# Kernel optimization log

Hardware: AMD Instinct MI355X
Metric: run time of the kernel (lower is better)

The kernel has to match this reference:

```python
import jax, jax.numpy as jnp
import numpy as np

N = 1 << 20
L, F, T = 16, 2, 1 << 19          # levels, feats/level, hashmap size
BASE, DESIRED = 16, 2048
PLANE_RES, PF = 512, 8
APP_COUNT, APP_DIM = 1024, 48
GEO = 15
_b = np.exp((np.log(DESIRED) - np.log(BASE)) / (L - 1))
RES = np.floor(BASE * _b ** np.arange(L)).astype(np.float32)   # per-level grid res
PRIMES = np.array([1, 2654435761, 805459861], dtype=np.uint32)
CORNERS = np.stack(np.meshgrid(*[[0, 1]] * 3, indexing='ij'), -1).reshape(8, 3)
PAIRS = np.array([[0, 1], [0, 2], [1, 2]])


def hash_encode(pos01, tables):
    # pos01: [N,3] in [0,1]; tables: [L,T,F]
    corners_u = jnp.asarray(CORNERS, jnp.uint32)
    corners_b = jnp.asarray(CORNERS, bool)
    primes = jnp.asarray(PRIMES)

    def level(table, R):
        p = pos01 * R                      # [N,3]
        pf = jnp.floor(p)
        fr = p - pf                        # trilinear weights
        pi = pf.astype(jnp.uint32)
        corner = pi[:, None, :] + corners_u            # [N,8,3]
        h = corner * primes                            # uint32 wraps (mod 2^32)
        idx = (h[..., 0] ^ h[..., 1] ^ h[..., 2]) & jnp.uint32(T - 1)
        w = jnp.prod(jnp.where(corners_b, fr[:, None, :], 1.0 - fr[:, None, :]), axis=-1)
        return jnp.einsum('nkf,nk->nf', table[idx], w)  # [N,F]

    feats = jax.vmap(level)(tables, jnp.asarray(RES))   # [L,N,F]
    return jnp.moveaxis(feats, 0, 1).reshape(pos01.shape[0], L * F)


def plane_encode(pos01, planes):
    # planes: [3, R, R, PF]; bilinear interp on (xy, xz, yz) projections
    outs = []
    for i in range(3):
        uv = pos01[:, PAIRS[i]] * (PLANE_RES - 1)
        uf = jnp.floor(uv)
        fr = uv - uf
        ui = jnp.clip(uf.astype(jnp.int32), 0, PLANE_RES - 2)
        u0, v0 = ui[:, 0], ui[:, 1]
        pl = planes[i]
        wu, wv = fr[:, 0:1], fr[:, 1:2]
        f = (pl[u0, v0] * (1 - wu) * (1 - wv) + pl[u0, v0 + 1] * (1 - wu) * wv
             + pl[u0 + 1, v0] * wu * (1 - wv) + pl[u0 + 1, v0 + 1] * wu * wv)
        outs.append(f)
    return jnp.concatenate(outs, -1)   # [N, 3*PF]


def sh_encode(d):
    # degree-4 real spherical harmonics (torch-ngp convention), d normalized
    x, y, z = d[:, 0], d[:, 1], d[:, 2]
    xx, yy, zz = x * x, y * y, z * z
    xy, yz, xz = x * y, y * z, x * z
    return jnp.stack([
        0.28209479177387814 * jnp.ones_like(x),
        -0.48860251190291987 * y, 0.48860251190291987 * z, -0.48860251190291987 * x,
        1.0925484305920792 * xy, -1.0925484305920792 * yz,
        0.94617469575755997 * zz - 0.31539156525252005,
        -1.0925484305920792 * xz, 0.5462742152960396 * (xx - yy),
        -0.5900435899266435 * y * (3 * xx - yy), 2.890611442640554 * xy * z,
        -0.4570457994644658 * y * (4 * zz - xx - yy),
        0.3731763325901154 * z * (2 * zz - 3 * xx - 3 * yy),
        -0.4570457994644658 * x * (4 * zz - xx - yy),
        1.445305721320277 * z * (xx - yy),
        -0.5900435899266435 * x * (xx - 3 * yy)], axis=-1)


def setup_inputs() -> dict:
    key = jax.random.key(0)
    ks = jax.random.split(key, 10)
    pos = jax.random.uniform(ks[0], (N, 3), jnp.float32, -1.0, 1.0)
    dirs = jax.random.normal(ks[1], (N, 3), jnp.float32)
    dirs = dirs / jnp.linalg.norm(dirs, axis=-1, keepdims=True)
    app = jax.random.randint(ks[2], (N, 1), 0, APP_COUNT).astype(jnp.float32)
    x = jnp.concatenate([pos, dirs, app], -1)
    hash_tables = jax.random.uniform(ks[3], (L, T, F), jnp.float32, -1e-4, 1e-4)
    planes = jax.random.normal(ks[4], (3, PLANE_RES, PLANE_RES, PF), jnp.float32) * 0.1
    embed_a = jax.random.normal(ks[5], (APP_COUNT, APP_DIM), jnp.float32)

    def lin(k, o, i):
        return jax.random.normal(k, (o, i), jnp.float32) * np.float32(np.sqrt(2.0 / i))
    return {
        'x': x, 'hash_tables': hash_tables, 'planes': planes, 'embed_a': embed_a,
        'w_sigma0': lin(ks[6], 64, L * F + 3 * PF),
        'w_sigma1': lin(ks[7], 1 + GEO, 64),
        'w_color0': lin(ks[8], 64, 16 + GEO + APP_DIM + 3 * PF),
        'w_color1': lin(ks[9], 64, 64),
        'w_color2': lin(jax.random.fold_in(key, 99), 3, 64),
    }


def reference(x, hash_tables, planes, embed_a, w_sigma0, w_sigma1, w_color0, w_color1, w_color2):
    pos01 = (x[:, :3] + 1.0) * 0.5            # bound = 1 -> [0,1]
    h = hash_encode(pos01, hash_tables)       # [N,32]
    pf = plane_encode(pos01, planes)          # [N,24]
    h = jnp.concatenate([h, pf], -1)
    h = jax.nn.relu(h @ w_sigma0.T)
    h = h @ w_sigma1.T                        # [N,16]
    sigma = jnp.exp(jnp.clip(h[..., 0], -15.0, 15.0))   # trunc_exp
    geo = h[..., 1:]
    d = x[:, 3:6]
    d = d / jnp.linalg.norm(d, axis=-1, keepdims=True)
    sh = sh_encode(d)                         # [N,16]
    a = embed_a[x[:, -1].astype(jnp.int32)]   # [N,48]
    hc = jnp.concatenate([sh, geo, a, pf], -1)
    hc = jax.nn.relu(hc @ w_color0.T)
    hc = jax.nn.relu(hc @ w_color1.T)
    color = jax.nn.sigmoid(hc @ w_color2.T)
    return jnp.concatenate([color, sigma[:, None]], -1)   # [N,4]
```

## Files before the change

### kernel.cpp

```cpp
#include <hip/hip_runtime.h>
#include <cmath>
#include <stdint.h>

#define NLEV  16
#define TSIZE (1u<<19)
#define PRES  512
#define PFD   8
#define HID   64
#define LDSH  72

struct ResArr { float v[NLEV]; };

typedef __attribute__((ext_vector_type(8))) short short8v;
typedef __attribute__((ext_vector_type(4))) float f32x4;

__device__ __forceinline__ float4 ld4(const float* p){ return *reinterpret_cast<const float4*>(p); }

__device__ __forceinline__ uint16_t f2bf(float f){
    uint32_t u = __float_as_uint(f);
    uint32_t r = (u + 0x7FFFu + ((u>>16)&1u)) >> 16;
    return (uint16_t)r;
}
__device__ __forceinline__ float bf2f(uint32_t h){ return __uint_as_float(h<<16); }

#define AXPY64(A, WPTR, V) do { const float* _w=(WPTR); const float _v=(V); \
  _Pragma("unroll") \
  for (int _o=0;_o<64;_o+=4){ float4 _w4=ld4(_w+_o); \
    A[_o+0]=fmaf(_w4.x,_v,A[_o+0]); A[_o+1]=fmaf(_w4.y,_v,A[_o+1]); \
    A[_o+2]=fmaf(_w4.z,_v,A[_o+2]); A[_o+3]=fmaf(_w4.w,_v,A[_o+3]); } } while(0)

__device__ __forceinline__ void plane_enc(const float* __restrict__ planes,
                                          float p0, float p1, float p2, float* pfv)
{
#pragma unroll
    for (int i=0;i<3;i++){
        float ua = (i==2? p1 : p0)*511.f;
        float va = (i==0? p1 : p2)*511.f;
        float uf=floorf(ua), vf=floorf(va);
        float wu=ua-uf, wv=va-vf;
        int u0=(int)uf; u0 = u0<0?0:(u0>510?510:u0);
        int v0=(int)vf; v0 = v0<0?0:(v0>510?510:v0);
        const float* pl = planes + ((size_t)i*PRES*PRES + (size_t)(u0*PRES+v0))*PFD;
        float4 a0=ld4(pl),              a1=ld4(pl+4);
        float4 b0=ld4(pl+PFD),          b1=ld4(pl+PFD+4);
        float4 c0=ld4(pl+PRES*PFD),     c1=ld4(pl+PRES*PFD+4);
        float4 d0=ld4(pl+PRES*PFD+PFD), d1=ld4(pl+PRES*PFD+PFD+4);
        float w00=(1.f-wu)*(1.f-wv), w01=(1.f-wu)*wv, w10=wu*(1.f-wv), w11=wu*wv;
        pfv[i*8+0]=a0.x*w00+b0.x*w01+c0.x*w10+d0.x*w11;
        pfv[i*8+1]=a0.y*w00+b0.y*w01+c0.y*w10+d0.y*w11;
        pfv[i*8+2]=a0.z*w00+b0.z*w01+c0.z*w10+d0.z*w11;
        pfv[i*8+3]=a0.w*w00+b0.w*w01+c0.w*w10+d0.w*w11;
        pfv[i*8+4]=a1.x*w00+b1.x*w01+c1.x*w10+d1.x*w11;
        pfv[i*8+5]=a1.y*w00+b1.y*w01+c1.y*w10+d1.y*w11;
        pfv[i*8+6]=a1.z*w00+b1.z*w01+c1.z*w10+d1.z*w11;
        pfv[i*8+7]=a1.w*w00+b1.w*w01+c1.w*w10+d1.w*w11;
    }
}

__global__ void nerf_krepack(const float2* __restrict__ tabs,
                             uint32_t* __restrict__ tabs_bf, int total)
{
    int i = blockIdx.x*256 + threadIdx.x;
    if (i < total){
        float2 t = tabs[i];
        tabs_bf[i] = (uint32_t)f2bf(t.x) | ((uint32_t)f2bf(t.y)<<16);
    }
}

__global__ void nerf_kprep(const float* __restrict__ x, float4* __restrict__ pp, int npts)
{
    int n = blockIdx.x*256 + threadIdx.x;
    if (n < npts){
        const float* xr = x + (size_t)n*7;
        pp[n] = make_float4((xr[0]+1.f)*0.5f, (xr[1]+1.f)*0.5f, (xr[2]+1.f)*0.5f, xr[6]);
    }
}

__global__ __launch_bounds__(256, 2)
void nerf_k0b(const float4* __restrict__ pp,
              const uint32_t* __restrict__ tabs_bf,
              uint32_t* __restrict__ feat,
              ResArr res, int npts, int lvl_base)
{
    int bid   = blockIdx.x;
    int level = lvl_base + (bid & 7);
    int chunk = bid >> 3;
    int base_n = chunk*2048 + threadIdx.x;
    float R = res.v[level];
    const uint32_t* tab = tabs_bf + (size_t)level*TSIZE;

    uint32_t g[8][8];
    float rx[8], ry[8], rz[8];
#pragma unroll
    for (int q=0;q<8;q++){
        int n = base_n + q*256;
        int nc = (n < npts) ? n : 0;
        float4 p = pp[nc];
        float ax=p.x*R, ay=p.y*R, az=p.z*R;
        float fx=floorf(ax), fy=floorf(ay), fz=floorf(az);
        rx[q]=ax-fx; ry[q]=ay-fy; rz[q]=az-fz;
        uint32_t ix=(uint32_t)fx, iy=(uint32_t)fy, iz=(uint32_t)fz;
        uint32_t hx0=ix,             hx1=ix+1u;
        uint32_t hy0=iy*2654435761u, hy1=(iy+1u)*2654435761u;
        uint32_t hz0=iz*805459861u,  hz1=(iz+1u)*805459861u;
#pragma unroll
        for (int c=0;c<8;c++){
            uint32_t idx = (((c&4)?hx1:hx0) ^ ((c&2)?hy1:hy0) ^ ((c&1)?hz1:hz0)) & (TSIZE-1u);
            g[q][c] = tab[idx];
        }
    }
#pragma unroll
    for (int q=0;q<8;q++){
        float wx0=1.f-rx[q], wy0=1.f-ry[q], wz0=1.f-rz[q];
        float f0=0.f, f1=0.f;
#pragma unroll
        for (int c=0;c<8;c++){
            float w = ((c&4)?rx[q]:wx0)*((c&2)?ry[q]:wy0)*((c&1)?rz[q]:wz0);
            f0 = fmaf(w, bf2f(g[q][c] & 0xFFFFu), f0);
            f1 = fmaf(w, bf2f(g[q][c] >> 16),     f1);
        }
        int n = base_n + q*256;
        if (n < npts) feat[(size_t)level*npts + n] = (uint32_t)f2bf(f0) | ((uint32_t)f2bf(f1)<<16);
    }
}

__global__ __launch_bounds__(256, 2)
void nerf_k0(const float* __restrict__ x,
             const float* __restrict__ hash_tables,
             uint32_t* __restrict__ feat,
             ResArr res, int npts, int lvl_base)
{
    int bid   = blockIdx.x;
    int level = lvl_base + (bid & 7);
    int chunk = bid >> 3;
    int n0 = chunk*512 + threadIdx.x;
    int n1 = n0 + 256;
    float R = res.v[level];
    const float2* tab = reinterpret_cast<const float2*>(hash_tables) + (size_t)level*TSIZE;

    bool v0ok = (n0 < npts), v1ok = (n1 < npts);

    float p0a=0,p1a=0,p2a=0, p0b=0,p1b=0,p2b=0;
    if (v0ok){ const float* xr = x + (size_t)n0*7;
        p0a=(xr[0]+1.f)*0.5f; p1a=(xr[1]+1.f)*0.5f; p2a=(xr[2]+1.f)*0.5f; }
    if (v1ok){ const float* xr = x + (size_t)n1*7;
        p0b=(xr[0]+1.f)*0.5f; p1b=(xr[1]+1.f)*0.5f; p2b=(xr[2]+1.f)*0.5f; }

    float axa=p0a*R, aya=p1a*R, aza=p2a*R;
    float fxa=floorf(axa), fya=floorf(aya), fza=floorf(aza);
    float rxa=axa-fxa, rya=aya-fya, rza=aza-fza;
    uint32_t ixa=(uint32_t)fxa, iya=(uint32_t)fya, iza=(uint32_t)fza;
    uint32_t hx0a=ixa,             hx1a=ixa+1u;
    uint32_t hy0a=iya*2654435761u, hy1a=(iya+1u)*2654435761u;
    uint32_t hz0a=iza*805459861u,  hz1a=(iza+1u)*805459861u;

    float axb=p0b*R, ayb=p1b*R, azb=p2b*R;
    float fxb=floorf(axb), fyb=floorf(ayb), fzb=floorf(azb);
    float rxb=axb-fxb, ryb=ayb-fyb, rzb=azb-fzb;
    uint32_t ixb=(uint32_t)fxb, iyb=(uint32_t)fyb, izb=(uint32_t)fzb;
    uint32_t hx0b=ixb,             hx1b=ixb+1u;
    uint32_t hy0b=iyb*2654435761u, hy1b=(iyb+1u)*2654435761u;
    uint32_t hz0b=izb*805459861u,  hz1b=(izb+1u)*805459861u;

    float2 ta[8], tb[8];
#pragma unroll
    for (int c=0;c<8;c++){
        uint32_t idx = (((c&4)?hx1a:hx0a) ^ ((c&2)?hy1a:hy0a) ^ ((c&1)?hz1a:hz0a)) & (TSIZE-1u);
        ta[c] = tab[idx];
    }
#pragma unroll
    for (int c=0;c<8;c++){
        uint32_t idx = (((c&4)?hx1b:hx0b) ^ ((c&2)?hy1b:hy0b) ^ ((c&1)?hz1b:hz0b)) & (TSIZE-1u);
        tb[c] = tab[idx];
    }

    float wxa0=1.f-rxa, wya0=1.f-rya, wza0=1.f-rza;
    float f0a=0.f, f1a=0.f;
#pragma unroll
    for (int c=0;c<8;c++){
        float w = ((c&4)?rxa:wxa0)*((c&2)?rya:wya0)*((c&1)?rza:wza0);
        f0a = fmaf(w,ta[c].x,f0a); f1a = fmaf(w,ta[c].y,f1a);
    }
    float wxb0=1.f-rxb, wyb0=1.f-ryb, wzb0=1.f-rzb;
    float f0b=0.f, f1b=0.f;
#pragma unroll
    for (int c=0;c<8;c++){
        float w = ((c&4)?rxb:wxb0)*((c&2)?ryb:wyb0)*((c&1)?rzb:wzb0);
        f0b = fmaf(w,tb[c].x,f0b); f1b = fmaf(w,tb[c].y,f1b);
    }

    size_t base = (size_t)level*npts;
    if (v0ok) feat[base+n0] = (uint32_t)f2bf(f0a) | ((uint32_t)f2bf(f1a)<<16);
    if (v1ok) feat[base+n1] = (uint32_t)f2bf(f0b) | ((uint32_t)f2bf(f1b)<<16);
}

__global__ void nerf_ktrans(const float* __restrict__ w_sigma0,
                            const float* __restrict__ w_sigma1,
                            const float* __restrict__ w_color0,
                            const float* __restrict__ w_color1,
                            const float* __restrict__ w_color2,
                            float* __restrict__ t_s0, float* __restrict__ t_s1,
                            float* __restrict__ t_c2,
                            short* __restrict__ c0Bhi, short* __restrict__ c0Blo,
                            short* __restrict__ c1Bhi, short* __restrict__ c1Blo,
                            short* __restrict__ s0Bhi, short* __restrict__ s0Blo,
                            short* __restrict__ s1Bhi, short* __restrict__ s1Blo,
                            short* __restrict__ c2Bhi, short* __restrict__ c2Blo)
{
    int tid = threadIdx.x;
    for (int i=tid;i<56*64; i+=256){ int k=i>>6,o=i&63; t_s0[i]=w_sigma0[o*56+k]; }
    for (int i=tid;i<64*16; i+=256){ int k=i>>4,j=i&15; t_s1[i]=w_sigma1[j*64+k]; }
    for (int i=tid;i<64*4;  i+=256){ int k=i>>2,o=i&3;  t_c2[i]=(o<3)?w_color2[o*64+k]:0.f; }

    for (int idx=tid; idx<4096; idx+=256){
        int nt = idx >> 10;
        int r1 = idx & 1023;
        int ks = r1 >> 9;
        int r2 = r1 & 511;
        int l  = r2 >> 3;
        int i  = r2 & 7;
        int out = nt*16 + (l & 15);
        int kk  = ks*32 + (l >> 4)*8 + i;
        float w0 = 0.f;
        if (kk < 31)       w0 = w_color0[out*103 + kk];
        else if (kk < 55)  w0 = w_color0[out*103 + kk + 48];
        uint16_t h0 = f2bf(w0);
        uint16_t l0 = f2bf(w0 - bf2f(h0));
        c0Bhi[idx] = (short)h0; c0Blo[idx] = (short)l0;
        float w1 = w_color1[out*64 + kk];
        uint16_t h1 = f2bf(w1);
        uint16_t l1 = f2bf(w1 - bf2f(h1));
        c1Bhi[idx] = (short)h1; c1Blo[idx] = (short)l1;
        float ws = (kk < 56) ? w_sigma0[out*56 + kk] : 0.f;
        uint16_t hs = f2bf(ws);
        uint16_t ls = f2bf(ws - bf2f(hs));
        s0Bhi[idx] = (short)hs; s0Blo[idx] = (short)ls;
    }
    for (int idx=tid; idx<1024; idx+=256){
        int ks = idx >> 9;
        int r2 = idx & 511;
        int l  = r2 >> 3;
        int i  = r2 & 7;
        int out = l & 15;
        int kk  = ks*32 + (l >> 4)*8 + i;
        float w = w_sigma1[out*64 + kk];
        uint16_t h = f2bf(w);
        s1Bhi[idx] = (short)h; s1Blo[idx] = (short)f2bf(w - bf2f(h));
        float wc = (out < 3) ? w_color2[out*64 + kk] : 0.f;
        uint16_t hc2 = f2bf(wc);
        c2Bhi[idx] = (short)hc2; c2Blo[idx] = (short)f2bf(wc - bf2f(hc2));
    }
}

__global__ void nerf_kpre(const float* __restrict__ embed_a,
                          const float* __restrict__ w_color0,
                          float* __restrict__ app_pre)
{
    int a = blockIdx.x;
    int o = threadIdx.x;
    const float* er = embed_a + (size_t)a*48;
    const float* wr = w_color0 + (size_t)o*103 + 31;
    float s = 0.f;
#pragma unroll
    for (int j=0;j<48;j++) s = fmaf(er[j], wr[j], s);
    app_pre[(size_t)a*64 + o] = s;
}

__global__ __launch_bounds__(256, 2)
void nerf_k1s(const float* __restrict__ x,
              const float* __restrict__ planes,
              uint32_t* __restrict__ feat,
              const float* __restrict__ wT_s0,
              const float* __restrict__ wT_s1,
              int npts)
{
    int n = blockIdx.x*256 + threadIdx.x;
    if (n >= npts) return;

    uint32_t fl[NLEV];
#pragma unroll
    for (int l=0;l<NLEV;l++) fl[l] = feat[(size_t)l*npts + n];

    float acc[HID];
#pragma unroll
    for (int o=0;o<HID;o++) acc[o]=0.f;

#pragma unroll
    for (int l=0;l<NLEV;l++){
        float f0 = bf2f(fl[l] & 0xFFFFu);
        float f1 = bf2f(fl[l] >> 16);
        AXPY64(acc, &wT_s0[(2*l+0)*64], f0);
        AXPY64(acc, &wT_s0[(2*l+1)*64], f1);
    }

    const float* xr = x + (size_t)n*7;
    float p0=(xr[0]+1.f)*0.5f, p1=(xr[1]+1.f)*0.5f, p2=(xr[2]+1.f)*0.5f;
    float pfv[24];
    plane_enc(planes, p0, p1, p2, pfv);
#pragma unroll
    for (int j=0;j<24;j++){
        AXPY64(acc, &wT_s0[(32+j)*64], pfv[j]);
    }

    float h1[16];
#pragma unroll
    for (int j=0;j<16;j++) h1[j]=0.f;
#pragma unroll
    for (int k=0;k<HID;k++){
        float v = fmaxf(acc[k], 0.f);
        const float* wr = &wT_s1[k*16];
#pragma unroll
        for (int j=0;j<16;j+=4){
            float4 w=ld4(wr+j);
            h1[j+0]=fmaf(w.x,v,h1[j+0]); h1[j+1]=fmaf(w.y,v,h1[j+1]);
            h1[j+2]=fmaf(w.z,v,h1[j+2]); h1[j+3]=fmaf(w.w,v,h1[j+3]);
        }
    }
    float sg = fminf(fmaxf(h1[0], -15.f), 15.f);
    float sigma = expf(sg);

#pragma unroll
    for (int l=0;l<15;l++) feat[(size_t)l*npts + n] = __float_as_uint(h1[l+1]);
    feat[(size_t)15*npts + n] = __float_as_uint(sigma);
}

__global__ __launch_bounds__(64, 1)
void nerf_k2m(const float* __restrict__ x,
              const float* __restrict__ planes,
              const uint32_t* __restrict__ feat,
              const float* __restrict__ app_pre,
              const short* __restrict__ c0Bhi, const short* __restrict__ c0Blo,
              const short* __restrict__ c1Bhi, const short* __restrict__ c1Blo,
              const float* __restrict__ t_c2,
              float* __restrict__ out, int npts)
{
    __shared__ uint16_t ldsA[2*64*LDSH];
    __shared__ int      lds_ai[64];

    const int l = threadIdx.x;
    int n = blockIdx.x*64 + l;
    bool ok = (n < npts);
    int nc = ok ? n : (npts-1);
    const float* xr = x + (size_t)nc*7;

    {
        float av[55];
        float dx=xr[3], dy=xr[4], dz=xr[5];
        float nrm = sqrtf(dx*dx+dy*dy+dz*dz);
        float sx=dx/nrm, sy=dy/nrm, sz=dz/nrm;
        float xx=sx*sx, yy=sy*sy, zz=sz*sz, xyv=sx*sy, yzv=sy*sz, xzv=sx*sz;
        av[0]=0.28209479177387814f;
        av[1]=-0.48860251190291987f*sy;
        av[2]= 0.48860251190291987f*sz;
        av[3]=-0.48860251190291987f*sx;
        av[4]= 1.0925484305920792f*xyv;
        av[5]=-1.0925484305920792f*yzv;
        av[6]= 0.94617469575756f*zz-0.31539156525252005f;
        av[7]=-1.0925484305920792f*xzv;
        av[8]= 0.5462742152960396f*(xx-yy);
        av[9]=-0.5900435899266435f*sy*(3.f*xx-yy);
        av[10]=2.890611442640554f*xyv*sz;
        av[11]=-0.4570457994644658f*sy*(4.f*zz-xx-yy);
        av[12]=0.3731763325901154f*sz*(2.f*zz-3.f*xx-3.f*yy);
        av[13]=-0.4570457994644658f*sx*(4.f*zz-xx-yy);
        av[14]=1.445305721320277f*sz*(xx-yy);
        av[15]=-0.5900435899266435f*sx*(xx-3.f*yy);
#pragma unroll
        for (int j=0;j<15;j++) av[16+j] = __uint_as_float(feat[(size_t)j*npts + nc]);
        float pfv[24];
        plane_enc(planes, (xr[0]+1.f)*0.5f, (xr[1]+1.f)*0.5f, (xr[2]+1.f)*0.5f, pfv);
#pragma unroll
        for (int j=0;j<24;j++) av[31+j] = pfv[j];

        uint16_t* rh = &ldsA[l*LDSH];
        uint16_t* rl = &ldsA[64*LDSH + l*LDSH];
#pragma unroll
        for (int kk=0; kk<64; kk++){
            float a = (kk<55) ? av[kk] : 0.f;
            uint16_t hi = f2bf(a);
            uint16_t lo = f2bf(a - bf2f(hi));
            rh[kk] = hi; rl[kk] = lo;
        }
        lds_ai[l] = (int)xr[6];
    }
    __syncthreads();

    f32x4 acc[4][4];
    {
        const int lq = l >> 4, lr = l & 15;
#pragma unroll
        for (int mt=0; mt<4; mt++){
#pragma unroll
            for (int r=0; r<4; r++){
                int ai = lds_ai[mt*16 + lq*4 + r];
                const float* ap = app_pre + (size_t)ai*64 + lr;
#pragma unroll
                for (int nt=0; nt<4; nt++)
                    acc[mt][nt][r] = ap[nt*16];
            }
        }
    }
    {
        const int lq = l >> 4, lr = l & 15;
#pragma unroll
        for (int ks=0; ks<2; ks++){
            short8v ah[4], al[4];
#pragma unroll
            for (int mt=0; mt<4; mt++){
                const uint16_t* ph = &ldsA[(mt*16+lr)*LDSH + ks*32 + lq*8];
                ah[mt] = *reinterpret_cast<const short8v*>(ph);
                al[mt] = *reinterpret_cast<const short8v*>(ph + 64*LDSH);
            }
#pragma unroll
            for (int nt=0; nt<4; nt++){
                short8v bh = *reinterpret_cast<const short8v*>(&c0Bhi[(nt*2+ks)*512 + l*8]);
                short8v bl = *reinterpret_cast<const short8v*>(&c0Blo[(nt*2+ks)*512 + l*8]);
#pragma unroll
                for (int mt=0; mt<4; mt++){
                    acc[mt][nt] = __builtin_amdgcn_mfma_f32_16x16x32_bf16(ah[mt], bh, acc[mt][nt], 0,0,0);
                    acc[mt][nt] = __builtin_amdgcn_mfma_f32_16x16x32_bf16(ah[mt], bl, acc[mt][nt], 0,0,0);
                    acc[mt][nt] = __builtin_amdgcn_mfma_f32_16x16x32_bf16(al[mt], bh, acc[mt][nt], 0,0,0);
                }
            }
        }
    }
    __syncthreads();

    {
        const int lq = l >> 4, lr = l & 15;
#pragma unroll
        for (int mt=0; mt<4; mt++){
#pragma unroll
            for (int nt=0; nt<4; nt++){
#pragma unroll
                for (int r=0; r<4; r++){
                    float v = fmaxf(acc[mt][nt][r], 0.f);
                    uint16_t hi = f2bf(v);
                    uint16_t lo = f2bf(v - bf2f(hi));
                    int pt = mt*16 + lq*4 + r;
                    int ch = nt*16 + lr;
                    ldsA[pt*LDSH + ch] = hi;
                    ldsA[64*LDSH + pt*LDSH + ch] = lo;
                }
            }
        }
    }
    __syncthreads();

    {
        const int lq = l >> 4, lr = l & 15;
#pragma unroll
        for (int mt=0; mt<4; mt++)
#pragma unroll
            for (int nt=0; nt<4; nt++){
                acc[mt][nt][0]=0.f; acc[mt][nt][1]=0.f; acc[mt][nt][2]=0.f; acc[mt][nt][3]=0.f;
            }
#pragma unroll
        for (int ks=0; ks<2; ks++){
            short8v ah[4], al[4];
#pragma unroll
            for (int mt=0; mt<4; mt++){
                const uint16_t* ph = &ldsA[(mt*16+lr)*LDSH + ks*32 + lq*8];
                ah[mt] = *reinterpret_cast<const short8v*>(ph);
                al[mt] = *reinterpret_cast<const short8v*>(ph + 64*LDSH);
            }
#pragma unroll
            for (int nt=0; nt<4; nt++){
                short8v bh = *reinterpret_cast<const short8v*>(&c1Bhi[(nt*2+ks)*512 + l*8]);
                short8v bl = *reinterpret_cast<const short8v*>(&c1Blo[(nt*2+ks)*512 + l*8]);
#pragma unroll
                for (int mt=0; mt<4; mt++){
                    acc[mt][nt] = __builtin_amdgcn_mfma_f32_16x16x32_bf16(ah[mt], bh, acc[mt][nt], 0,0,0);
                    acc[mt][nt] = __builtin_amdgcn_mfma_f32_16x16x32_bf16(ah[mt], bl, acc[mt][nt], 0,0,0);
                    acc[mt][nt] = __builtin_amdgcn_mfma_f32_16x16x32_bf16(al[mt], bh, acc[mt][nt], 0,0,0);
                }
            }
        }
    }
    __syncthreads();

    {
        float* ldsF = reinterpret_cast<float*>(ldsA);
        const int lq = l >> 4, lr = l & 15;
#pragma unroll
        for (int mt=0; mt<4; mt++){
#pragma unroll
            for (int nt=0; nt<4; nt++){
#pragma unroll
                for (int r=0; r<4; r++){
                    int pt = mt*16 + lq*4 + r;
                    int ch = nt*16 + lr;
                    ldsF[pt*66 + ch] = fmaxf(acc[mt][nt][r], 0.f);
                }
            }
        }
        __syncthreads();

        float c0=0.f, c1=0.f, c2=0.f;
        const float* row = &ldsF[l*66];
#pragma unroll
        for (int ch=0; ch<64; ch++){
            float v = row[ch];
            float4 w = ld4(&t_c2[ch*4]);
            c0 = fmaf(w.x, v, c0);
            c1 = fmaf(w.y, v, c1);
            c2 = fmaf(w.z, v, c2);
        }
        if (ok){
            float sigma = __uint_as_float(feat[(size_t)15*npts + n]);
            float4 o4;
            o4.x = 1.f/(1.f+expf(-c0));
            o4.y = 1.f/(1.f+expf(-c1));
            o4.z = 1.f/(1.f+expf(-c2));
            o4.w = sigma;
            *reinterpret_cast<float4*>(out + (size_t)n*4) = o4;
        }
    }
}

__global__ __launch_bounds__(64, 1)
void nerf_k12m(const float* __restrict__ x,
               const float* __restrict__ planes,
               const uint32_t* __restrict__ feat,
               const float* __restrict__ app_pre,
               const short* __restrict__ s0Bhi, const short* __restrict__ s0Blo,
               const short* __restrict__ s1Bhi, const short* __restrict__ s1Blo,
               const short* __restrict__ c0Bhi, const short* __restrict__ c0Blo,
               const short* __restrict__ c1Bhi, const short* __restrict__ c1Blo,
               const short* __restrict__ c2Bhi, const short* __restrict__ c2Blo,
               float* __restrict__ out, int npts)
{
    __shared__ uint16_t ldsA[64*LDSH];
    __shared__ uint16_t ldsB[64*LDSH];
    __shared__ float    obuf[64*4];
    __shared__ float    sig[64];
    __shared__ int      lds_ai[64];

    const int l = threadIdx.x;
    const int lq = l >> 4, lr = l & 15;
    int n = blockIdx.x*64 + l;
    bool ok = (n < npts);
    int nc = ok ? n : (npts-1);
    const float* xr = x + (size_t)nc*7;

    float pfv[24];
    float sh[16];
    {
        float dx=xr[3], dy=xr[4], dz=xr[5];
        float nrm = sqrtf(dx*dx+dy*dy+dz*dz);
        float sx=dx/nrm, sy=dy/nrm, sz=dz/nrm;
        float xx=sx*sx, yy=sy*sy, zz=sz*sz, xyv=sx*sy, yzv=sy*sz, xzv=sx*sz;
        sh[0]=0.28209479177387814f;
        sh[1]=-0.48860251190291987f*sy;
        sh[2]= 0.48860251190291987f*sz;
        sh[3]=-0.48860251190291987f*sx;
        sh[4]= 1.0925484305920792f*xyv;
        sh[5]=-1.0925484305920792f*yzv;
        sh[6]= 0.94617469575756f*zz-0.31539156525252005f;
        sh[7]=-1.0925484305920792f*xzv;
        sh[8]= 0.5462742152960396f*(xx-yy);
        sh[9]=-0.5900435899266435f*sy*(3.f*xx-yy);
        sh[10]=2.890611442640554f*xyv*sz;
        sh[11]=-0.4570457994644658f*sy*(4.f*zz-xx-yy);
        sh[12]=0.3731763325901154f*sz*(2.f*zz-3.f*xx-3.f*yy);
        sh[13]=-0.4570457994644658f*sx*(4.f*zz-xx-yy);
        sh[14]=1.445305721320277f*sz*(xx-yy);
        sh[15]=-0.5900435899266435f*sx*(xx-3.f*yy);
        plane_enc(planes, (xr[0]+1.f)*0.5f, (xr[1]+1.f)*0.5f, (xr[2]+1.f)*0.5f, pfv);
        lds_ai[l] = (int)xr[6];
    }

    {
        uint16_t* rh = &ldsA[l*LDSH];
        uint16_t* rl = &ldsB[l*LDSH];
#pragma unroll
        for (int lv=0; lv<16; lv++){
            *reinterpret_cast<uint32_t*>(&rh[2*lv]) = feat[(size_t)lv*npts + nc];
            *reinterpret_cast<uint32_t*>(&rl[2*lv]) = 0u;
        }
#pragma unroll
        for (int j=0;j<24;j++){
            float a = pfv[j];
            uint16_t hi = f2bf(a);
            rh[32+j] = hi;
            rl[32+j] = f2bf(a - bf2f(hi));
        }
#pragma unroll
        for (int j=56;j<64;j++){ rh[j]=0; rl[j]=0; }
    }
    __syncthreads();

    f32x4 acc[4][4];
#pragma unroll
    for (int mt=0; mt<4; mt++)
#pragma unroll
        for (int nt=0; nt<4; nt++){
            acc[mt][nt][0]=0.f; acc[mt][nt][1]=0.f; acc[mt][nt][2]=0.f; acc[mt][nt][3]=0.f;
        }
#pragma unroll
    for (int ks=0; ks<2; ks++){
        short8v ah[4], al[4];
#pragma unroll
        for (int mt=0; mt<4; mt++){
            ah[mt] = *reinterpret_cast<const short8v*>(&ldsA[(mt*16+lr)*LDSH + ks*32 + lq*8]);
            al[mt] = *reinterpret_cast<const short8v*>(&ldsB[(mt*16+lr)*LDSH + ks*32 + lq*8]);
        }
#pragma unroll
        for (int nt=0; nt<4; nt++){
            short8v bh = *reinterpret_cast<const short8v*>(&s0Bhi[(nt*2+ks)*512 + l*8]);
            short8v bl = *reinterpret_cast<const short8v*>(&s0Blo[(nt*2+ks)*512 + l*8]);
#pragma unroll
            for (int mt=0; mt<4; mt++){
                acc[mt][nt] = __builtin_amdgcn_mfma_f32_16x16x32_bf16(ah[mt], bh, acc[mt][nt], 0,0,0);
                acc[mt][nt] = __builtin_amdgcn_mfma_f32_16x16x32_bf16(ah[mt], bl, acc[mt][nt], 0,0,0);
                if (ks==1)
                    acc[mt][nt] = __builtin_amdgcn_mfma_f32_16x16x32_bf16(al[mt], bh, acc[mt][nt], 0,0,0);
            }
        }
    }
    __syncthreads();

#pragma unroll
    for (int mt=0; mt<4; mt++){
#pragma unroll
        for (int nt=0; nt<4; nt++){
#pragma unroll
            for (int r=0; r<4; r++){
                float v = fmaxf(acc[mt][nt][r], 0.f);
                uint16_t hi = f2bf(v);
                int pt = mt*16 + lq*4 + r;
                int ch = nt*16 + lr;
                ldsA[pt*LDSH + ch] = hi;
                ldsB[pt*LDSH + ch] = f2bf(v - bf2f(hi));
            }
        }
    }
    __syncthreads();

    f32x4 acc2[4];
#pragma unroll
    for (int mt=0; mt<4; mt++){ acc2[mt][0]=0.f; acc2[mt][1]=0.f; acc2[mt][2]=0.f; acc2[mt][3]=0.f; }
#pragma unroll
    for (int ks=0; ks<2; ks++){
        short8v bh = *reinterpret_cast<const short8v*>(&s1Bhi[ks*512 + l*8]);
        short8v bl = *reinterpret_cast<const short8v*>(&s1Blo[ks*512 + l*8]);
#pragma unroll
        for (int mt=0; mt<4; mt++){
            short8v ah = *reinterpret_cast<const short8v*>(&ldsA[(mt*16+lr)*LDSH + ks*32 + lq*8]);
            short8v al = *reinterpret_cast<const short8v*>(&ldsB[(mt*16+lr)*LDSH + ks*32 + lq*8]);
            acc2[mt] = __builtin_amdgcn_mfma_f32_16x16x32_bf16(ah, bh, acc2[mt], 0,0,0);
            acc2[mt] = __builtin_amdgcn_mfma_f32_16x16x32_bf16(ah, bl, acc2[mt], 0,0,0);
            acc2[mt] = __builtin_amdgcn_mfma_f32_16x16x32_bf16(al, bh, acc2[mt], 0,0,0);
        }
    }
    __syncthreads();

    {
        uint16_t* rh = &ldsA[l*LDSH];
        uint16_t* rl = &ldsB[l*LDSH];
#pragma unroll
        for (int j=0;j<16;j++){
            float a = sh[j];
            uint16_t hi = f2bf(a);
            rh[j] = hi; rl[j] = f2bf(a - bf2f(hi));
        }
#pragma unroll
        for (int j=0;j<24;j++){
            float a = pfv[j];
            uint16_t hi = f2bf(a);
            rh[31+j] = hi; rl[31+j] = f2bf(a - bf2f(hi));
        }
#pragma unroll
        for (int j=55;j<64;j++){ rh[j]=0; rl[j]=0; }

        int ch = lr;
#pragma unroll
        for (int mt=0; mt<4; mt++){
#pragma unroll
            for (int r=0; r<4; r++){
                int pt = mt*16 + lq*4 + r;
                float v = acc2[mt][r];
                if (ch == 0){
                    sig[pt] = v;
                } else {
                    uint16_t hi = f2bf(v);
                    ldsA[pt*LDSH + 16 + (ch-1)] = hi;
                    ldsB[pt*LDSH + 16 + (ch-1)] = f2bf(v - bf2f(hi));
                }
            }
        }
    }
    __syncthreads();

#pragma unroll
    for (int mt=0; mt<4; mt++){
#pragma unroll
        for (int r=0; r<4; r++){
            int ai = lds_ai[mt*16 + lq*4 + r];
            const float* ap = app_pre + (size_t)ai*64 + lr;
#pragma unroll
            for (int nt=0; nt<4; nt++)
                acc[mt][nt][r] = ap[nt*16];
        }
    }
#pragma unroll
    for (int ks=0; ks<2; ks++){
        short8v ah[4], al[4];
#pragma unroll
        for (int mt=0; mt<4; mt++){
            ah[mt] = *reinterpret_cast<const short8v*>(&ldsA[(mt*16+lr)*LDSH + ks*32 + lq*8]);
            al[mt] = *reinterpret_cast<const short8v*>(&ldsB[(mt*16+lr)*LDSH + ks*32 + lq*8]);
        }
#pragma unroll
        for (int nt=0; nt<4; nt++){
            short8v bh = *reinterpret_cast<const short8v*>(&c0Bhi[(nt*2+ks)*512 + l*8]);
            short8v bl = *reinterpret_cast<const short8v*>(&c0Blo[(nt*2+ks)*512 + l*8]);
#pragma unroll
            for (int mt=0; mt<4; mt++){
                acc[mt][nt] = __builtin_amdgcn_mfma_f32_16x16x32_bf16(ah[mt], bh, acc[mt][nt], 0,0,0);
                acc[mt][nt] = __builtin_amdgcn_mfma_f32_16x16x32_bf16(ah[mt], bl, acc[mt][nt], 0,0,0);
                acc[mt][nt] = __builtin_amdgcn_mfma_f32_16x16x32_bf16(al[mt], bh, acc[mt][nt], 0,0,0);
            }
        }
    }
    __syncthreads();

#pragma unroll
    for (int mt=0; mt<4; mt++){
#pragma unroll
        for (int nt=0; nt<4; nt++){
#pragma unroll
            for (int r=0; r<4; r++){
                float v = fmaxf(acc[mt][nt][r], 0.f);
                uint16_t hi = f2bf(v);
                int pt = mt*16 + lq*4 + r;
                int ch = nt*16 + lr;
                ldsA[pt*LDSH + ch] = hi;
                ldsB[pt*LDSH + ch] = f2bf(v - bf2f(hi));
            }
        }
    }
    __syncthreads();

#pragma unroll
    for (int mt=0; mt<4; mt++)
#pragma unroll
        for (int nt=0; nt<4; nt++){
            acc[mt][nt][0]=0.f; acc[mt][nt][1]=0.f; acc[mt][nt][2]=0.f; acc[mt][nt][3]=0.f;
        }
#pragma unroll
    for (int ks=0; ks<2; ks++){
        short8v ah[4], al[4];
#pragma unroll
        for (int mt=0; mt<4; mt++){
            ah[mt] = *reinterpret_cast<const short8v*>(&ldsA[(mt*16+lr)*LDSH + ks*32 + lq*8]);
            al[mt] = *reinterpret_cast<const short8v*>(&ldsB[(mt*16+lr)*LDSH + ks*32 + lq*8]);
        }
#pragma unroll
        for (int nt=0; nt<4; nt++){
            short8v bh = *reinterpret_cast<const short8v*>(&c1Bhi[(nt*2+ks)*512 + l*8]);
            short8v bl = *reinterpret_cast<const short8v*>(&c1Blo[(nt*2+ks)*512 + l*8]);
#pragma unroll
            for (int mt=0; mt<4; mt++){
                acc[mt][nt] = __builtin_amdgcn_mfma_f32_16x16x32_bf16(ah[mt], bh, acc[mt][nt], 0,0,0);
                acc[mt][nt] = __builtin_amdgcn_mfma_f32_16x16x32_bf16(ah[mt], bl, acc[mt][nt], 0,0,0);
                acc[mt][nt] = __builtin_amdgcn_mfma_f32_16x16x32_bf16(al[mt], bh, acc[mt][nt], 0,0,0);
            }
        }
    }
    __syncthreads();

#pragma unroll
    for (int mt=0; mt<4; mt++){
#pragma unroll
        for (int nt=0; nt<4; nt++){
#pragma unroll
            for (int r=0; r<4; r++){
                float v = fmaxf(acc[mt][nt][r], 0.f);
                uint16_t hi = f2bf(v);
                int pt = mt*16 + lq*4 + r;
                int ch = nt*16 + lr;
                ldsA[pt*LDSH + ch] = hi;
                ldsB[pt*LDSH + ch] = f2bf(v - bf2f(hi));
            }
        }
    }
    __syncthreads();

    f32x4 acc3[4];
#pragma unroll
    for (int mt=0; mt<4; mt++){ acc3[mt][0]=0.f; acc3[mt][1]=0.f; acc3[mt][2]=0.f; acc3[mt][3]=0.f; }
#pragma unroll
    for (int ks=0; ks<2; ks++){
        short8v bh = *reinterpret_cast<const short8v*>(&c2Bhi[ks*512 + l*8]);
        short8v bl = *reinterpret_cast<const short8v*>(&c2Blo[ks*512 + l*8]);
#pragma unroll
        for (int mt=0; mt<4; mt++){
            short8v ah = *reinterpret_cast<const short8v*>(&ldsA[(mt*16+lr)*LDSH + ks*32 + lq*8]);
            short8v al = *reinterpret_cast<const short8v*>(&ldsB[(mt*16+lr)*LDSH + ks*32 + lq*8]);
            acc3[mt] = __builtin_amdgcn_mfma_f32_16x16x32_bf16(ah, bh, acc3[mt], 0,0,0);
            acc3[mt] = __builtin_amdgcn_mfma_f32_16x16x32_bf16(ah, bl, acc3[mt], 0,0,0);
            acc3[mt] = __builtin_amdgcn_mfma_f32_16x16x32_bf16(al, bh, acc3[mt], 0,0,0);
        }
    }
    if (lr < 3){
#pragma unroll
        for (int mt=0; mt<4; mt++){
#pragma unroll
            for (int r=0; r<4; r++){
                obuf[(mt*16 + lq*4 + r)*4 + lr] = acc3[mt][r];
            }
        }
    }
    __syncthreads();

    if (ok){
        float sg = fminf(fmaxf(sig[l], -15.f), 15.f);
        float4 o4;
        o4.x = 1.f/(1.f+expf(-obuf[l*4+0]));
        o4.y = 1.f/(1.f+expf(-obuf[l*4+1]));
        o4.z = 1.f/(1.f+expf(-obuf[l*4+2]));
        o4.w = expf(sg);
        *reinterpret_cast<float4*>(out + (size_t)n*4) = o4;
    }
}

__global__ __launch_bounds__(256, 1)
void nerf_fwd(const float* __restrict__ x,
              const float* __restrict__ hash_tables,
              const float* __restrict__ planes,
              const float* __restrict__ embed_a,
              const float* __restrict__ w_sigma0,
              const float* __restrict__ w_sigma1,
              const float* __restrict__ w_color0,
              const float* __restrict__ w_color1,
              const float* __restrict__ w_color2,
              float* __restrict__ out,
              ResArr res, int npts)
{
    __shared__ float s_ws0T[56*64];
    __shared__ float s_ws1T[64*16];
    __shared__ float s_wc0T[103*64];
    __shared__ float s_wc1T[64*64];
    __shared__ float s_wc2T[64*4];

    for (int i = threadIdx.x; i < 56*64;  i += 256){ int k=i>>6, o=i&63; s_ws0T[i] = w_sigma0[o*56+k]; }
    for (int i = threadIdx.x; i < 64*16;  i += 256){ int k=i>>4, j=i&15; s_ws1T[i] = w_sigma1[j*64+k]; }
    for (int i = threadIdx.x; i < 103*64; i += 256){ int k=i>>6, o=i&63; s_wc0T[i] = w_color0[o*103+k]; }
    for (int i = threadIdx.x; i < 64*64;  i += 256){ int k=i>>6, o=i&63; s_wc1T[i] = w_color1[o*64+k]; }
    for (int i = threadIdx.x; i < 64*4;   i += 256){ int k=i>>2, o=i&3;  s_wc2T[i] = (o<3)? w_color2[o*64+k] : 0.f; }
    __syncthreads();

    int n = blockIdx.x*256 + threadIdx.x;
    if (n >= npts) return;

    const float* xr = x + (size_t)n*7;
    float px=xr[0], py=xr[1], pz=xr[2];
    float dx=xr[3], dy=xr[4], dz=xr[5];
    float appf = xr[6];
    float p0=(px+1.f)*0.5f, p1=(py+1.f)*0.5f, p2=(pz+1.f)*0.5f;

    float acc[HID];
#pragma unroll
    for (int o=0;o<HID;o++) acc[o]=0.f;

    const float2* tabs = reinterpret_cast<const float2*>(hash_tables);
    for (int l=0; l<NLEV; l++){
        float R = res.v[l];
        float ax=p0*R, ay=p1*R, az=p2*R;
        float fx=floorf(ax), fy=floorf(ay), fz=floorf(az);
        float rx=ax-fx, ry=ay-fy, rz=az-fz;
        uint32_t ix=(uint32_t)fx, iy=(uint32_t)fy, iz=(uint32_t)fz;
        const float2* tab = tabs + (size_t)l*TSIZE;
        uint32_t hx0=ix,               hx1=ix+1u;
        uint32_t hy0=iy*2654435761u,   hy1=(iy+1u)*2654435761u;
        uint32_t hz0=iz*805459861u,    hz1=(iz+1u)*805459861u;
        float wx0=1.f-rx, wx1=rx, wy0=1.f-ry, wy1=ry, wz0=1.f-rz, wz1=rz;
        float f0=0.f, f1=0.f;
#pragma unroll
        for (int c=0;c<8;c++){
            uint32_t hxx=(c&4)?hx1:hx0;
            uint32_t hyy=(c&2)?hy1:hy0;
            uint32_t hzz=(c&1)?hz1:hz0;
            uint32_t idx=(hxx^hyy^hzz)&(TSIZE-1u);
            float2 t = tab[idx];
            float w = ((c&4)?wx1:wx0)*((c&2)?wy1:wy0)*((c&1)?wz1:wz0);
            f0 = fmaf(w,t.x,f0);
            f1 = fmaf(w,t.y,f1);
        }
        AXPY64(acc, &s_ws0T[(2*l+0)*64], f0);
        AXPY64(acc, &s_ws0T[(2*l+1)*64], f1);
    }

    float pfv[24];
    plane_enc(planes, p0, p1, p2, pfv);
#pragma unroll
    for (int j=0;j<24;j++){
        AXPY64(acc, &s_ws0T[(32+j)*64], pfv[j]);
    }

    float h1[16];
#pragma unroll
    for (int j=0;j<16;j++) h1[j]=0.f;
#pragma unroll
    for (int k=0;k<HID;k++){
        float v = fmaxf(acc[k], 0.f);
        const float* wr = &s_ws1T[k*16];
#pragma unroll
        for (int j=0;j<16;j+=4){
            float4 w=ld4(wr+j);
            h1[j+0]=fmaf(w.x,v,h1[j+0]); h1[j+1]=fmaf(w.y,v,h1[j+1]);
            h1[j+2]=fmaf(w.z,v,h1[j+2]); h1[j+3]=fmaf(w.w,v,h1[j+3]);
        }
    }
    float sg = fminf(fmaxf(h1[0], -15.f), 15.f);
    float sigma = expf(sg);

#pragma unroll
    for (int o=0;o<HID;o++) acc[o]=0.f;

    float nrm = sqrtf(dx*dx+dy*dy+dz*dz);
    float sx=dx/nrm, sy=dy/nrm, sz=dz/nrm;
    float xx=sx*sx, yy=sy*sy, zz=sz*sz, xyv=sx*sy, yzv=sy*sz, xzv=sx*sz;
    float sh[16];
    sh[0]=0.28209479177387814f;
    sh[1]=-0.48860251190291987f*sy;
    sh[2]= 0.48860251190291987f*sz;
    sh[3]=-0.48860251190291987f*sx;
    sh[4]= 1.0925484305920792f*xyv;
    sh[5]=-1.0925484305920792f*yzv;
    sh[6]= 0.94617469575756f*zz-0.31539156525252005f;
    sh[7]=-1.0925484305920792f*xzv;
    sh[8]= 0.5462742152960396f*(xx-yy);
    sh[9]=-0.5900435899266435f*sy*(3.f*xx-yy);
    sh[10]=2.890611442640554f*xyv*sz;
    sh[11]=-0.4570457994644658f*sy*(4.f*zz-xx-yy);
    sh[12]=0.3731763325901154f*sz*(2.f*zz-3.f*xx-3.f*yy);
    sh[13]=-0.4570457994644658f*sx*(4.f*zz-xx-yy);
    sh[14]=1.445305721320277f*sz*(xx-yy);
    sh[15]=-0.5900435899266435f*sx*(xx-3.f*yy);
#pragma unroll
    for (int k=0;k<16;k++){
        AXPY64(acc, &s_wc0T[k*64], sh[k]);
    }
#pragma unroll
    for (int j=0;j<15;j++){
        AXPY64(acc, &s_wc0T[(16+j)*64], h1[1+j]);
    }
    {
        int ai = (int)appf;
        const float* ar = embed_a + (size_t)ai*48;
        for (int q=0;q<12;q++){
            float4 av = ld4(ar + q*4);
            const float* wc = &s_wc0T[(31+q*4)*64];
            AXPY64(acc, wc,       av.x);
            AXPY64(acc, wc+64,    av.y);
            AXPY64(acc, wc+128,   av.z);
            AXPY64(acc, wc+192,   av.w);
        }
    }
#pragma unroll
    for (int j=0;j<24;j++){
        AXPY64(acc, &s_wc0T[(79+j)*64], pfv[j]);
    }

    float acc2[HID];
#pragma unroll
    for (int o=0;o<HID;o++) acc2[o]=0.f;
#pragma unroll
    for (int k=0;k<HID;k++){
        float v = fmaxf(acc[k], 0.f);
        AXPY64(acc2, &s_wc1T[k*64], v);
    }

    float c0a=0.f, c1a=0.f, c2a=0.f;
#pragma unroll
    for (int k=0;k<HID;k++){
        float v = fmaxf(acc2[k], 0.f);
        float4 w = ld4(&s_wc2T[k*4]);
        c0a=fmaf(w.x,v,c0a); c1a=fmaf(w.y,v,c1a); c2a=fmaf(w.z,v,c2a);
    }
    float4 o4;
    o4.x = 1.f/(1.f+expf(-c0a));
    o4.y = 1.f/(1.f+expf(-c1a));
    o4.z = 1.f/(1.f+expf(-c2a));
    o4.w = sigma;
    *reinterpret_cast<float4*>(out + (size_t)n*4) = o4;
}

extern "C" void kernel_launch(void* const* d_in, const int* in_sizes, int n_in,
                              void* d_out, int out_size, void* d_ws, size_t ws_size,
                              hipStream_t stream) {
    const float* x        = (const float*)d_in[0];
    const float* ht       = (const float*)d_in[1];
    const float* planes   = (const float*)d_in[2];
    const float* embed_a  = (const float*)d_in[3];
    const float* w_sigma0 = (const float*)d_in[4];
    const float* w_sigma1 = (const float*)d_in[5];
    const float* w_color0 = (const float*)d_in[6];
    const float* w_color1 = (const float*)d_in[7];
    const float* w_color2 = (const float*)d_in[8];
    float* out = (float*)d_out;

    int npts = in_sizes[0] / 7;

    ResArr res;
    double b = exp((log(2048.0) - log(16.0)) / 15.0);
    for (int l=0; l<NLEV; l++)
        res.v[l] = (float)floor(16.0 * pow(b, (double)l));

    const size_t OFF_S0  = 0;
    const size_t OFF_S1  = OFF_S0 + 56*64*4;
    const size_t OFF_C2  = OFF_S1 + 64*16*4;
    const size_t OFF_AP  = OFF_C2 + 64*4*4;
    const size_t OFF_B0H = OFF_AP + 1024*64*4;
    const size_t OFF_B0L = OFF_B0H + 4096*2;
    const size_t OFF_B1H = OFF_B0L + 4096*2;
    const size_t OFF_B1L = OFF_B1H + 4096*2;
    const size_t OFF_SB0H= OFF_B1L + 4096*2;
    const size_t OFF_SB0L= OFF_SB0H + 4096*2;
    const size_t OFF_SB1H= OFF_SB0L + 4096*2;
    const size_t OFF_SB1L= OFF_SB1H + 1024*2;
    const size_t OFF_C2BH= OFF_SB1L + 1024*2;
    const size_t OFF_C2BL= OFF_C2BH + 1024*2;
    const size_t OFF_SMALL_END = OFF_C2BL + 1024*2;
    size_t feat_bytes = (size_t)npts * 16 * sizeof(uint32_t);
    size_t pp_bytes   = (size_t)npts * 16;
    size_t tb_bytes   = (size_t)16 * TSIZE * 4;

    const size_t OFF_PP   = OFF_SMALL_END;
    const size_t OFF_TB   = OFF_PP + pp_bytes;
    const size_t OFF_FEAT2= OFF_TB + tb_bytes;
    const size_t OFF_FEAT1= OFF_SMALL_END;

    bool full_path = (ws_size >= OFF_FEAT2 + feat_bytes);
    bool mid_path  = (ws_size >= OFF_FEAT1 + feat_bytes);

    if (full_path || mid_path) {
        char* base = (char*)d_ws;
        float* t_s0  = (float*)(base + OFF_S0);
        float* t_s1  = (float*)(base + OFF_S1);
        float* t_c2  = (float*)(base + OFF_C2);
        float* a_pre = (float*)(base + OFF_AP);
        short* c0Bhi = (short*)(base + OFF_B0H);
        short* c0Blo = (short*)(base + OFF_B0L);
        short* c1Bhi = (short*)(base + OFF_B1H);
        short* c1Blo = (short*)(base + OFF_B1L);
        short* s0Bhi = (short*)(base + OFF_SB0H);
        short* s0Blo = (short*)(base + OFF_SB0L);
        short* s1Bhi = (short*)(base + OFF_SB1H);
        short* s1Blo = (short*)(base + OFF_SB1L);
        short* c2Bhi = (short*)(base + OFF_C2BH);
        short* c2Blo = (short*)(base + OFF_C2BL);

        hipLaunchKernelGGL(nerf_ktrans, dim3(1), dim3(256), 0, stream,
                           w_sigma0, w_sigma1, w_color0, w_color1, w_color2,
                           t_s0, t_s1, t_c2, c0Bhi, c0Blo, c1Bhi, c1Blo,
                           s0Bhi, s0Blo, s1Bhi, s1Blo, c2Bhi, c2Blo);
        hipLaunchKernelGGL(nerf_kpre, dim3(1024), dim3(64), 0, stream,
                           embed_a, w_color0, a_pre);

        if (full_path) {
            float4*   pp      = (float4*)(base + OFF_PP);
            uint32_t* tabs_bf = (uint32_t*)(base + OFF_TB);
            uint32_t* feat    = (uint32_t*)(base + OFF_FEAT2);

            int total = 16 * (int)TSIZE;
            hipLaunchKernelGGL(nerf_krepack, dim3((total+255)/256), dim3(256), 0, stream,
                               (const float2*)ht, tabs_bf, total);
            hipLaunchKernelGGL(nerf_kprep, dim3((npts+255)/256), dim3(256), 0, stream,
                               x, pp, npts);

            int chunks = (npts + 2047) / 2048;
            hipLaunchKernelGGL(nerf_k0b, dim3(8*chunks), dim3(256), 0, stream,
                               pp, tabs_bf, feat, res, npts, 0);
            hipLaunchKernelGGL(nerf_k0b, dim3(8*chunks), dim3(256), 0, stream,
                               pp, tabs_bf, feat, res, npts, 8);

            int gm = (npts + 63) / 64;
            hipLaunchKernelGGL(nerf_k12m, dim3(gm), dim3(64), 0, stream,
                               x, planes, feat, a_pre,
                               s0Bhi, s0Blo, s1Bhi, s1Blo,
                               c0Bhi, c0Blo, c1Bhi, c1Blo, c2Bhi, c2Blo, out, npts);
        } else {
            uint32_t* feat = (uint32_t*)(base + OFF_FEAT1);
            int chunks = (npts + 511) / 512;
            hipLaunchKernelGGL(nerf_k0, dim3(8*chunks), dim3(256), 0, stream,
                               x, ht, feat, res, npts, 0);
            hipLaunchKernelGGL(nerf_k0, dim3(8*chunks), dim3(256), 0, stream,
                               x, ht, feat, res, npts, 8);
            int g = (npts + 255) / 256;
            hipLaunchKernelGGL(nerf_k1s, dim3(g), dim3(256), 0, stream,
                               x, planes, feat, t_s0, t_s1, npts);
            int gm = (npts + 63) / 64;
            hipLaunchKernelGGL(nerf_k2m, dim3(gm), dim3(64), 0, stream,
                               x, planes, feat, a_pre,
                               c0Bhi, c0Blo, c1Bhi, c1Blo, t_c2, out, npts);
        }
    } else {
        int grid = (npts + 255) / 256;
        hipLaunchKernelGGL(nerf_fwd, dim3(grid), dim3(256), 0, stream,
                           x, ht, planes, embed_a,
                           w_sigma0, w_sigma1, w_color0, w_color1, w_color2,
                           out, res, npts);
    }
}
```

Before: 685.9 us.

## Merge small prep kernels, relax k0b launch bounds, truncate bf16 hi split

Merges the table repack and position prep into one launch, and folds the appearance precompute into the weight-transform kernel, which cuts launch count and inter-kernel gaps. Changes nerf_k0b launch bounds from 2 to 1 waves per SIMD hint, giving the compiler more registers at the cost of occupancy. Replaces round-to-nearest with truncation for the high bf16 part of the hi/lo split in the MLP kernel, saving ALU work. The low part absorbs the larger residual, so accuracy should be roughly preserved.

```diff
diff --git a/kernel.cpp b/kernel.cpp
--- a/kernel.cpp
+++ b/kernel.cpp
@@ -22,6 +22,8 @@
     return (uint16_t)r;
 }
 __device__ __forceinline__ float bf2f(uint32_t h){ return __uint_as_float(h<<16); }
+__device__ __forceinline__ uint16_t f2bf_hi(float f){ return (uint16_t)(__float_as_uint(f) >> 16); }
+__device__ __forceinline__ float resid(float f, uint16_t hi){ return f - __uint_as_float((uint32_t)hi << 16); }
 
 #define AXPY64(A, WPTR, V) do { const float* _w=(WPTR); const float _v=(V); \
   _Pragma("unroll") \
@@ -58,25 +60,26 @@
 }
 
 __global__ void nerf_krepack(const float2* __restrict__ tabs,
-                             uint32_t* __restrict__ tabs_bf, int total)
+                             uint32_t* __restrict__ tabs_bf, int total,
+                             const float* __restrict__ x, float4* __restrict__ pp, int npts)
 {
-    int i = blockIdx.x*256 + threadIdx.x;
-    if (i < total){
-        float2 t = tabs[i];
-        tabs_bf[i] = (uint32_t)f2bf(t.x) | ((uint32_t)f2bf(t.y)<<16);
+    int nb_rep = (total + 255) / 256;
+    if ((int)blockIdx.x < nb_rep){
+        int i = blockIdx.x*256 + threadIdx.x;
+        if (i < total){
+            float2 t = tabs[i];
+            tabs_bf[i] = (uint32_t)f2bf(t.x) | ((uint32_t)f2bf(t.y)<<16);
+        }
+    } else {
+        int n = (blockIdx.x - nb_rep)*256 + threadIdx.x;
+        if (n < npts){
+            const float* xr = x + (size_t)n*7;
+            pp[n] = make_float4((xr[0]+1.f)*0.5f, (xr[1]+1.f)*0.5f, (xr[2]+1.f)*0.5f, xr[6]);
+        }
     }
 }
 
-__global__ void nerf_kprep(const float* __restrict__ x, float4* __restrict__ pp, int npts)
-{
-    int n = blockIdx.x*256 + threadIdx.x;
-    if (n < npts){
-        const float* xr = x + (size_t)n*7;
-        pp[n] = make_float4((xr[0]+1.f)*0.5f, (xr[1]+1.f)*0.5f, (xr[2]+1.f)*0.5f, xr[6]);
-    }
-}
-
-__global__ __launch_bounds__(256, 2)
+__global__ __launch_bounds__(256, 1)
 void nerf_k0b(const float4* __restrict__ pp,
               const uint32_t* __restrict__ tabs_bf,
               uint32_t* __restrict__ feat,
@@ -205,8 +208,24 @@
                             short* __restrict__ c1Bhi, short* __restrict__ c1Blo,
                             short* __restrict__ s0Bhi, short* __restrict__ s0Blo,
                             short* __restrict__ s1Bhi, short* __restrict__ s1Blo,
-                            short* __restrict__ c2Bhi, short* __restrict__ c2Blo)
+                            short* __restrict__ c2Bhi, short* __restrict__ c2Blo,
+                            const float* __restrict__ embed_a,
+                            float* __restrict__ app_pre)
 {
+    if (blockIdx.x > 0){
+        int a = blockIdx.x - 1;
+        int o = threadIdx.x;
+        if (o < 64){
+            const float* er = embed_a + (size_t)a*48;
+            const float* wr = w_color0 + (size_t)o*103 + 31;
+            float s = 0.f;
+#pragma unroll
+            for (int j=0;j<48;j++) s = fmaf(er[j], wr[j], s);
+            app_pre[(size_t)a*64 + o] = s;
+        }
+        return;
+    }
+
     int tid = threadIdx.x;
     for (int i=tid;i<56*64; i+=256){ int k=i>>6,o=i&63; t_s0[i]=w_sigma0[o*56+k]; }
     for (int i=tid;i<64*16; i+=256){ int k=i>>4,j=i&15; t_s1[i]=w_sigma1[j*64+k]; }
@@ -250,20 +269,6 @@
         uint16_t hc2 = f2bf(wc);
         c2Bhi[idx] = (short)hc2; c2Blo[idx] = (short)f2bf(wc - bf2f(hc2));
     }
-}
-
-__global__ void nerf_kpre(const float* __restrict__ embed_a,
-                          const float* __restrict__ w_color0,
-                          float* __restrict__ app_pre)
-{
-    int a = blockIdx.x;
-    int o = threadIdx.x;
-    const float* er = embed_a + (size_t)a*48;
-    const float* wr = w_color0 + (size_t)o*103 + 31;
-    float s = 0.f;
-#pragma unroll
-    for (int j=0;j<48;j++) s = fmaf(er[j], wr[j], s);
-    app_pre[(size_t)a*64 + o] = s;
 }
 
 __global__ __launch_bounds__(256, 2)
@@ -581,9 +586,9 @@
 #pragma unroll
         for (int j=0;j<24;j++){
             float a = pfv[j];
-            uint16_t hi = f2bf(a);
+            uint16_t hi = f2bf_hi(a);
             rh[32+j] = hi;
-            rl[32+j] = f2bf(a - bf2f(hi));
+            rl[32+j] = f2bf(resid(a, hi));
         }
 #pragma unroll
         for (int j=56;j<64;j++){ rh[j]=0; rl[j]=0; }
@@ -627,11 +632,11 @@
 #pragma unroll
             for (int r=0; r<4; r++){
                 float v = fmaxf(acc[mt][nt][r], 0.f);
-                uint16_t hi = f2bf(v);
+                uint16_t hi = f2bf_hi(v);
                 int pt = mt*16 + lq*4 + r;
                 int ch = nt*16 + lr;
                 ldsA[pt*LDSH + ch] = hi;
-                ldsB[pt*LDSH + ch] = f2bf(v - bf2f(hi));
+                ldsB[pt*LDSH + ch] = f2bf(resid(v, hi));
             }
         }
     }
@@ -661,14 +666,14 @@
 #pragma unroll
         for (int j=0;j<16;j++){
             float a = sh[j];
-            uint16_t hi = f2bf(a);
-            rh[j] = hi; rl[j] = f2bf(a - bf2f(hi));
+            uint16_t hi = f2bf_hi(a);
+            rh[j] = hi; rl[j] = f2bf(resid(a, hi));
         }
 #pragma unroll
         for (int j=0;j<24;j++){
             float a = pfv[j];
-            uint16_t hi = f2bf(a);
-            rh[31+j] = hi; rl[31+j] = f2bf(a - bf2f(hi));
+            uint16_t hi = f2bf_hi(a);
+            rh[31+j] = hi; rl[31+j] = f2bf(resid(a, hi));
         }
 #pragma unroll
         for (int j=55;j<64;j++){ rh[j]=0; rl[j]=0; }
@@ -683,9 +688,9 @@
                 if (ch == 0){
                     sig[pt] = v;
                 } else {
-                    uint16_t hi = f2bf(v);
+                    uint16_t hi = f2bf_hi(v);
                     ldsA[pt*LDSH + 16 + (ch-1)] = hi;
-                    ldsB[pt*LDSH + 16 + (ch-1)] = f2bf(v - bf2f(hi));
+                    ldsB[pt*LDSH + 16 + (ch-1)] = f2bf(resid(v, hi));
                 }
             }
         }
@@ -732,11 +737,11 @@
 #pragma unroll
             for (int r=0; r<4; r++){
                 float v = fmaxf(acc[mt][nt][r], 0.f);
-                uint16_t hi = f2bf(v);
+                uint16_t hi = f2bf_hi(v);
                 int pt = mt*16 + lq*4 + r;
                 int ch = nt*16 + lr;
                 ldsA[pt*LDSH + ch] = hi;
-                ldsB[pt*LDSH + ch] = f2bf(v - bf2f(hi));
+                ldsB[pt*LDSH + ch] = f2bf(resid(v, hi));
             }
         }
     }
@@ -777,11 +782,11 @@
 #pragma unroll
             for (int r=0; r<4; r++){
                 float v = fmaxf(acc[mt][nt][r], 0.f);
-                uint16_t hi = f2bf(v);
+                uint16_t hi = f2bf_hi(v);
                 int pt = mt*16 + lq*4 + r;
                 int ch = nt*16 + lr;
                 ldsA[pt*LDSH + ch] = hi;
-                ldsB[pt*LDSH + ch] = f2bf(v - bf2f(hi));
+                ldsB[pt*LDSH + ch] = f2bf(resid(v, hi));
             }
         }
     }
@@ -1053,12 +1058,11 @@
         short* c2Bhi = (short*)(base + OFF_C2BH);
         short* c2Blo = (short*)(base + OFF_C2BL);
 
-        hipLaunchKernelGGL(nerf_ktrans, dim3(1), dim3(256), 0, stream,
+        hipLaunchKernelGGL(nerf_ktrans, dim3(1025), dim3(256), 0, stream,
                            w_sigma0, w_sigma1, w_color0, w_color1, w_color2,
                            t_s0, t_s1, t_c2, c0Bhi, c0Blo, c1Bhi, c1Blo,
-                           s0Bhi, s0Blo, s1Bhi, s1Blo, c2Bhi, c2Blo);
-        hipLaunchKernelGGL(nerf_kpre, dim3(1024), dim3(64), 0, stream,
-                           embed_a, w_color0, a_pre);
+                           s0Bhi, s0Blo, s1Bhi, s1Blo, c2Bhi, c2Blo,
+                           embed_a, a_pre);
 
         if (full_path) {
             float4*   pp      = (float4*)(base + OFF_PP);
@@ -1066,10 +1070,10 @@
             uint32_t* feat    = (uint32_t*)(base + OFF_FEAT2);
 
             int total = 16 * (int)TSIZE;
-            hipLaunchKernelGGL(nerf_krepack, dim3((total+255)/256), dim3(256), 0, stream,
-                               (const float2*)ht, tabs_bf, total);
-            hipLaunchKernelGGL(nerf_kprep, dim3((npts+255)/256), dim3(256), 0, stream,
-                               x, pp, npts);
+            int nb_rep = (total + 255) / 256;
+            int nb_pp  = (npts + 255) / 256;
+            hipLaunchKernelGGL(nerf_krepack, dim3(nb_rep + nb_pp), dim3(256), 0, stream,
+                               (const float2*)ht, tabs_bf, total, x, pp, npts);
 
             int chunks = (npts + 2047) / 2048;
             hipLaunchKernelGGL(nerf_k0b, dim3(8*chunks), dim3(256), 0, stream,
```

Result: no change. 675.7 us (-1.5%).
